# Kernel optimization log

Hardware: AMD Instinct MI355X
Metric: run time of the kernel (lower is better)

## Reference

```python
import jax, jax.numpy as jnp
import numpy as np

N = 50000        # num_nodes = user + item
D = 128          # latdim
L = 3            # gnn layers
R = 16           # hyper_rank
E = 1600000      # nnz of ts_drp_adj


def setup_inputs() -> dict:
    key = jax.random.key(0)
    ks = jax.random.split(key, 13)
    s = 1.0 / np.sqrt(D)
    return {
        "adj_rows": jax.random.randint(ks[0], (E,), 0, N, dtype=jnp.int32),
        "adj_cols": jax.random.randint(ks[1], (E,), 0, N, dtype=jnp.int32),
        "adj_vals": jax.random.uniform(ks[2], (E,), jnp.float32) * 0.05,
        "node_feats": jax.random.normal(ks[3], (N, D), jnp.float32) * s,
        "gnn_W": jax.random.normal(ks[4], (L, D, D), jnp.float32) * s,
        "gnn_b": jax.random.normal(ks[5], (L, D), jnp.float32) * 0.01,
        "fc1_W": jax.random.normal(ks[6], (D, D), jnp.float32) * s,
        "fc1_b": jax.random.normal(ks[7], (D,), jnp.float32) * 0.01,
        "fcrow_W": jax.random.normal(ks[8], (N * R, D), jnp.float32) * s,
        "fcrow_b": jax.random.normal(ks[9], (N * R,), jnp.float32) * 0.01,
        "fccol_W": jax.random.normal(ks[10], (R * D, D), jnp.float32) * s,
        "fccol_b": jax.random.normal(ks[11], (R * D,), jnp.float32) * 0.01,
        "ini_embeds": jax.random.normal(ks[12], (N, D), jnp.float32) * s,
    }


def _spmm(rows, cols, vals, h):
    # out[i] = sum_{e: rows[e]==i} vals[e] * h[cols[e]]   -- sparse adj @ h
    return jax.ops.segment_sum(vals[:, None] * h[cols], rows, num_segments=N)


def reference(adj_rows, adj_cols, adj_vals, node_feats, gnn_W, gnn_b,
              fc1_W, fc1_b, fcrow_W, fcrow_b, fccol_W, fccol_b, ini_embeds):
    h = node_feats
    h_sum = h  # running sum of layer outputs (residual mean-pool)
    for l in range(L):
        agg = _spmm(adj_rows, adj_cols, adj_vals, h)           # (N, D)
        h = jax.nn.elu(agg @ gnn_W[l].T + gnn_b[l])            # linear + ELU
        h_sum = h_sum + h
    h_bar = h_sum / (L + 1)
    z = h_bar.mean(axis=0)                                     # (D,)
    # Hypernetwork: z -> low-rank W_u = W_row @ W_col
    hz = jax.nn.leaky_relu(z @ fc1_W.T + fc1_b, negative_slope=0.2)
    W_row = (hz @ fcrow_W.T + fcrow_b).reshape(N, R)
    W_col = (hz @ fccol_W.T + fccol_b).reshape(R, D)
    W_u = W_row @ W_col                                        # (N, D)
    tuned_emb = ini_embeds + W_u * ini_embeds
    return tuned_emb
```

## Files before the change

kernel.cpp:

```cpp
#include <hip/hip_runtime.h>
#include <hip/hip_bf16.h>
#include <math.h>

#define NN 50000
#define DD 128
#define LLAYERS 3
#define RR 16
#define EE 1600000

typedef unsigned int u32;

__device__ __forceinline__ float bflo(u32 u){ union{u32 i;float f;}a; a.i=u<<16; return a.f; }
__device__ __forceinline__ float bfhi(u32 u){ union{u32 i;float f;}a; a.i=u&0xffff0000u; return a.f; }
__device__ __forceinline__ u32 pack_bf2(float x, float y){
  union{float f;u32 i;}a,b; a.f=x; b.f=y;
  u32 xr = (a.i + 0x7fffu + ((a.i>>16)&1u)) >> 16;
  u32 yr = (b.i + 0x7fffu + ((b.i>>16)&1u)) & 0xffff0000u;
  return (xr & 0xffffu) | yr;
}

__global__ __launch_bounds__(256) void k_hist(const int* __restrict__ rows, int* __restrict__ cnt){
  int e = blockIdx.x*256 + threadIdx.x;
  if (e < EE) atomicAdd(&cnt[rows[e]], 1);
}

__global__ __launch_bounds__(256) void k_scanA(const int* __restrict__ cnt, int* __restrict__ bsum){
  __shared__ int s[256];
  int i = blockIdx.x*256 + threadIdx.x;
  int v = (i < NN) ? cnt[i] : 0;
  s[threadIdx.x] = v; __syncthreads();
  for (int off=128; off>0; off>>=1){
    if (threadIdx.x < off) s[threadIdx.x] += s[threadIdx.x+off];
    __syncthreads();
  }
  if (threadIdx.x==0) bsum[blockIdx.x] = s[0];
}

__global__ __launch_bounds__(256) void k_scanB(int* bsum){
  __shared__ int s[256];
  int t = threadIdx.x;
  int v = bsum[t];
  s[t] = v; __syncthreads();
  for (int off=1; off<256; off<<=1){
    int x = (t>=off) ? s[t-off] : 0; __syncthreads();
    s[t] += x; __syncthreads();
  }
  bsum[t] = s[t] - v;
}

__global__ __launch_bounds__(256) void k_scanC(const int* __restrict__ cnt, const int* __restrict__ bsum,
                        int* __restrict__ row_ptr, int* __restrict__ cursor){
  __shared__ int s[256];
  int t = threadIdx.x; int i = blockIdx.x*256 + t;
  int v = (i<NN)?cnt[i]:0;
  s[t]=v; __syncthreads();
  for (int off=1; off<256; off<<=1){
    int x=(t>=off)?s[t-off]:0; __syncthreads();
    s[t]+=x; __syncthreads();
  }
  if (i<NN){ int e = bsum[blockIdx.x] + s[t]-v; row_ptr[i]=e; cursor[i]=e; }
}

__global__ __launch_bounds__(256) void k_scatter(const int* __restrict__ rows, const int* __restrict__ cols,
                          const float* __restrict__ vals,
                          int* __restrict__ cursor, int2* __restrict__ colval){
  int e = blockIdx.x*256+threadIdx.x;
  if (e<EE){
    int r = rows[e];
    int p = atomicAdd(&cursor[r],1);
    int2 cv; cv.x = cols[e]; cv.y = __float_as_int(vals[e]);
    colval[p] = cv;
  }
}

__global__ __launch_bounds__(256) void k_init(const float4* __restrict__ nf, uint2* __restrict__ hbf,
                                              float* __restrict__ z){
  __shared__ float zp[128];
  int t = threadIdx.x;
  if (t < 128) zp[t] = 0.f;
  float a0=0.f,a1=0.f,a2=0.f,a3=0.f;
  for (int i = blockIdx.x*256 + t; i < NN*DD/4; i += gridDim.x*256){
    float4 v = nf[i];
    uint2 p; p.x = pack_bf2(v.x, v.y); p.y = pack_bf2(v.z, v.w);
    hbf[i] = p;
    a0 += v.x; a1 += v.y; a2 += v.z; a3 += v.w;
  }
  __syncthreads();
  int c = (t*4) & 127;
  atomicAdd(&zp[c],a0); atomicAdd(&zp[c+1],a1); atomicAdd(&zp[c+2],a2); atomicAdd(&zp[c+3],a3);
  __syncthreads();
  if (t < 128) atomicAdd(&z[((blockIdx.x&15)<<7) + t], zp[t]);
}

__global__ __launch_bounds__(256) void k_wT(const float* __restrict__ W, float* __restrict__ wT){
  int idx = blockIdx.x*256+threadIdx.x;
  int l = idx >> 14; int r = idx & 16383; int k = r >> 7; int j = r & 127;
  wT[(l<<14) + k*128 + j] = W[(l<<14) + j*128 + k];
}

__global__ __launch_bounds__(256) void k_layer(const int* __restrict__ row_ptr, const int* __restrict__ cnt,
                       const int2* __restrict__ colval,
                       const u32* __restrict__ hin, const float* __restrict__ wTl,
                       const float* __restrict__ bl,
                       u32* __restrict__ hout, float* __restrict__ z, int last){
  __shared__ float a_s[16*128];
  __shared__ float zp[128];
  int t = threadIdx.x;
  if (t < 128) zp[t] = 0.f;
  int i0 = blockIdx.x * 16;
  int lane = t & 63;
  int wv = t >> 6;
  int sub = lane >> 4, k = lane & 15;

  for (int r = 0; r < 4; ++r){
    int row = i0 + wv*4 + r;
    int base = row_ptr[row], n = cnt[row];
    float a0=0,a1=0,a2=0,a3=0,a4=0,a5=0,a6=0,a7=0;
    int p = sub;
    for (; p + 4 < n; p += 8){
      int2 cv0 = colval[base+p];
      int2 cv1 = colval[base+p+4];
      uint4 h0 = *(const uint4*)&hin[((size_t)(u32)cv0.x<<6) + (k<<2)];
      uint4 h1 = *(const uint4*)&hin[((size_t)(u32)cv1.x<<6) + (k<<2)];
      float v0 = __int_as_float(cv0.y);
      float v1 = __int_as_float(cv1.y);
      a0 = fmaf(v0, bflo(h0.x), a0); a1 = fmaf(v0, bfhi(h0.x), a1);
      a2 = fmaf(v0, bflo(h0.y), a2); a3 = fmaf(v0, bfhi(h0.y), a3);
      a4 = fmaf(v0, bflo(h0.z), a4); a5 = fmaf(v0, bfhi(h0.z), a5);
      a6 = fmaf(v0, bflo(h0.w), a6); a7 = fmaf(v0, bfhi(h0.w), a7);
      a0 = fmaf(v1, bflo(h1.x), a0); a1 = fmaf(v1, bfhi(h1.x), a1);
      a2 = fmaf(v1, bflo(h1.y), a2); a3 = fmaf(v1, bfhi(h1.y), a3);
      a4 = fmaf(v1, bflo(h1.z), a4); a5 = fmaf(v1, bfhi(h1.z), a5);
      a6 = fmaf(v1, bflo(h1.w), a6); a7 = fmaf(v1, bfhi(h1.w), a7);
    }
    if (p < n){
      int2 cv = colval[base+p];
      float v = __int_as_float(cv.y);
      uint4 hv = *(const uint4*)&hin[((size_t)(u32)cv.x<<6) + (k<<2)];
      a0 = fmaf(v, bflo(hv.x), a0); a1 = fmaf(v, bfhi(hv.x), a1);
      a2 = fmaf(v, bflo(hv.y), a2); a3 = fmaf(v, bfhi(hv.y), a3);
      a4 = fmaf(v, bflo(hv.z), a4); a5 = fmaf(v, bfhi(hv.z), a5);
      a6 = fmaf(v, bflo(hv.w), a6); a7 = fmaf(v, bfhi(hv.w), a7);
    }
    a0 += __shfl_xor(a0,16); a0 += __shfl_xor(a0,32);
    a1 += __shfl_xor(a1,16); a1 += __shfl_xor(a1,32);
    a2 += __shfl_xor(a2,16); a2 += __shfl_xor(a2,32);
    a3 += __shfl_xor(a3,16); a3 += __shfl_xor(a3,32);
    a4 += __shfl_xor(a4,16); a4 += __shfl_xor(a4,32);
    a5 += __shfl_xor(a5,16); a5 += __shfl_xor(a5,32);
    a6 += __shfl_xor(a6,16); a6 += __shfl_xor(a6,32);
    a7 += __shfl_xor(a7,16); a7 += __shfl_xor(a7,32);
    if (sub==0){
      float4 o0; o0.x=a0; o0.y=a1; o0.z=a2; o0.w=a3;
      float4 o1; o1.x=a4; o1.y=a5; o1.z=a6; o1.w=a7;
      *(float4*)&a_s[(wv*4+r)*128 + k*8] = o0;
      *(float4*)&a_s[(wv*4+r)*128 + k*8 + 4] = o1;
    }
  }
  __syncthreads();

  int jj = lane*2;
  float b0 = bl[jj], b1 = bl[jj+1];
  float acc[4][2];
  #pragma unroll
  for (int r=0;r<4;r++){ acc[r][0]=b0; acc[r][1]=b1; }
  #pragma unroll 4
  for (int kk=0;kk<128;kk++){
    float2 w2 = *(const float2*)&wTl[kk*128 + jj];
    #pragma unroll
    for (int r=0;r<4;r++){
      float a = a_s[(wv*4+r)*128 + kk];
      acc[r][0] = fmaf(a, w2.x, acc[r][0]);
      acc[r][1] = fmaf(a, w2.y, acc[r][1]);
    }
  }
  float zc0 = 0.f, zc1 = 0.f;
  #pragma unroll
  for (int r=0;r<4;r++){
    int row = i0 + wv*4 + r;
    float e0 = acc[r][0] > 0.f ? acc[r][0] : expm1f(acc[r][0]);
    float e1 = acc[r][1] > 0.f ? acc[r][1] : expm1f(acc[r][1]);
    zc0 += e0; zc1 += e1;
    if (!last)
      hout[(size_t)row*64 + (jj>>1)] = pack_bf2(e0, e1);
  }
  atomicAdd(&zp[jj], zc0); atomicAdd(&zp[jj+1], zc1);
  __syncthreads();
  if (t < 128) atomicAdd(&z[((blockIdx.x&15)<<7) + t], zp[t]);
}

__global__ __launch_bounds__(128) void k_hz(const float* __restrict__ z, const float* __restrict__ fc1W,
                     const float* __restrict__ fc1b, float* __restrict__ hz){
  __shared__ float zs[128];
  int j = threadIdx.x;
  float s = 0.f;
  #pragma unroll
  for (int q=0;q<16;q++) s += z[(q<<7) + j];
  zs[j] = s * (1.0f / (4.0f * (float)NN));
  __syncthreads();
  float acc = fc1b[j];
  const float* wr = &fc1W[j*128];
  #pragma unroll 8
  for (int k=0;k<128;k++)
    acc = fmaf(zs[k], wr[k], acc);
  hz[j] = acc >= 0.f ? acc : 0.2f*acc;
}

__global__ __launch_bounds__(256) void k_wcol(const float* __restrict__ hz, const float* __restrict__ W,
                       const float* __restrict__ b, float* __restrict__ wcol){
  __shared__ float hzs[128];
  int t = threadIdx.x;
  if (t < 128) hzs[t] = hz[t];
  __syncthreads();
  int m = blockIdx.x*256 + t;
  float acc = b[m];
  const float* wr = &W[(size_t)m*128];
  #pragma unroll 8
  for (int k=0;k<128;k++)
    acc = fmaf(hzs[k], wr[k], acc);
  wcol[m] = acc;
}

__global__ __launch_bounds__(256) void k_wrow(const float* __restrict__ hz, const float* __restrict__ W,
                       const float* __restrict__ b, float* __restrict__ wrow){
  int lane = threadIdx.x & 63;
  int sub = lane >> 5, k = lane & 31;
  float4 hk = *(const float4*)&hz[k*4];
  int wid = (blockIdx.x*blockDim.x + threadIdx.x) >> 6;
  int nw = (gridDim.x*blockDim.x) >> 6;
  const int NITER = NN*RR/2;
  for (int it = wid; it < NITER; it += nw){
    int row = it*2 + sub;
    float4 wv = *(const float4*)&W[(size_t)row*128 + k*4];
    float acc = wv.x*hk.x;
    acc = fmaf(wv.y, hk.y, acc);
    acc = fmaf(wv.z, hk.z, acc);
    acc = fmaf(wv.w, hk.w, acc);
    acc += __shfl_xor(acc,1); acc += __shfl_xor(acc,2);
    acc += __shfl_xor(acc,4); acc += __shfl_xor(acc,8);
    acc += __shfl_xor(acc,16);
    if (k==0) wrow[row] = acc + b[row];
  }
}

__global__ __launch_bounds__(256) void k_final(const float* __restrict__ ini, const float* __restrict__ wrow,
                        const float* __restrict__ wcol, float* __restrict__ out){
  __shared__ float wc[16*128];
  int t = threadIdx.x;
  ((float4*)wc)[t] = ((const float4*)wcol)[t];
  ((float4*)wc)[t+256] = ((const float4*)wcol)[t+256];
  __syncthreads();
  int gid = blockIdx.x*256 + t;
  int i = gid >> 5, k = gid & 31;
  float4 a; a.x=0.f; a.y=0.f; a.z=0.f; a.w=0.f;
  const float* wri = &wrow[(size_t)i*16];
  #pragma unroll
  for (int r=0;r<16;r++){
    float w = wri[r];
    const float4 c = *(const float4*)&wc[r*128 + k*4];
    a.x = fmaf(w, c.x, a.x); a.y = fmaf(w, c.y, a.y);
    a.z = fmaf(w, c.z, a.z); a.w = fmaf(w, c.w, a.w);
  }
  float4 e = *(const float4*)&ini[(size_t)i*128 + k*4];
  float4 o;
  o.x = e.x*(1.f+a.x); o.y = e.y*(1.f+a.y);
  o.z = e.z*(1.f+a.z); o.w = e.w*(1.f+a.w);
  *(float4*)&out[(size_t)i*128 + k*4] = o;
}

extern "C" void kernel_launch(void* const* d_in, const int* in_sizes, int n_in,
                              void* d_out, int out_size, void* d_ws, size_t ws_size,
                              hipStream_t stream) {
  const int* adj_rows = (const int*)d_in[0];
  const int* adj_cols = (const int*)d_in[1];
  const float* adj_vals = (const float*)d_in[2];
  const float* node_feats = (const float*)d_in[3];
  const float* gnn_W = (const float*)d_in[4];
  const float* gnn_b = (const float*)d_in[5];
  const float* fc1_W = (const float*)d_in[6];
  const float* fc1_b = (const float*)d_in[7];
  const float* fcrow_W = (const float*)d_in[8];
  const float* fcrow_b = (const float*)d_in[9];
  const float* fccol_W = (const float*)d_in[10];
  const float* fccol_b = (const float*)d_in[11];
  const float* ini = (const float*)d_in[12];
  float* out = (float*)d_out;

  char* w = (char*)d_ws;
  auto alloc = [&](size_t bytes)->void*{ void* p = (void*)w; w += (bytes + 255) & ~(size_t)255; return p; };
  u32*   hbf_a  = (u32*)  alloc((size_t)NN*DD*2);
  u32*   hbf_b  = (u32*)  alloc((size_t)NN*DD*2);
  int2*  colval = (int2*) alloc((size_t)EE*8);
  int*   cnt    = (int*)  alloc((size_t)NN*4);
  int*   row_ptr= (int*)  alloc((size_t)NN*4);
  int*   cursor = (int*)  alloc((size_t)NN*4);
  int*   bsum   = (int*)  alloc(256*4);
  float* wT     = (float*)alloc(3*128*128*4);
  float* zb     = (float*)alloc(16*128*4);
  float* hzb    = (float*)alloc(128*4);
  float* wcolb  = (float*)alloc(2048*4);
  float* wrowb  = (float*)alloc((size_t)NN*RR*4);

  hipMemsetAsync(cnt, 0, NN*4, stream);
  hipMemsetAsync(zb, 0, 16*128*4, stream);

  k_hist<<<EE/256, 256, 0, stream>>>(adj_rows, cnt);
  k_scanA<<<256, 256, 0, stream>>>(cnt, bsum);
  k_scanB<<<1, 256, 0, stream>>>(bsum);
  k_scanC<<<256, 256, 0, stream>>>(cnt, bsum, row_ptr, cursor);
  k_scatter<<<EE/256, 256, 0, stream>>>(adj_rows, adj_cols, adj_vals, cursor, colval);
  k_init<<<400, 256, 0, stream>>>((const float4*)node_feats, (uint2*)hbf_a, zb);
  k_wT<<<3*128*128/256, 256, 0, stream>>>(gnn_W, wT);

  const u32* hin = hbf_a; u32* hout = hbf_b;
  for (int l=0; l<LLAYERS; ++l){
    k_layer<<<NN/16, 256, 0, stream>>>(row_ptr, cnt, colval, hin, wT + l*16384,
                                       gnn_b + l*128, hout, zb, (l==LLAYERS-1) ? 1 : 0);
    const u32* tmp = hin; hin = hout; hout = (u32*)tmp;
  }

  k_hz<<<1, 128, 0, stream>>>(zb, fc1_W, fc1_b, hzb);
  k_wcol<<<8, 256, 0, stream>>>(hzb, fccol_W, fccol_b, wcolb);
  k_wrow<<<2048, 256, 0, stream>>>(hzb, fcrow_W, fcrow_b, wrowb);
  k_final<<<NN*32/256, 256, 0, stream>>>(ini, wrowb, wcolb, out);
}
```

Measured before the change: 1.111 ms.

## Pad CSR rows to multiples of eight and software-pipeline SpMM gathers

Each row segment in the CSR arrays is padded to a multiple of 8 with zero-valued entries (column 0, value 0), plus a tail pad after the last row. The gather loop then needs no bounds check or remainder path. The inner SpMM loop is software-pipelined, prefetching colval two iterations ahead and feature rows one iteration ahead to hide gather latency. The cost is about 1.6x more colval storage at worst, an extra padding kernel, and wasted FMAs and gathers on padded slots.

```diff
diff --git a/kernel.cpp b/kernel.cpp
--- a/kernel.cpp
+++ b/kernel.cpp
@@ -27,7 +27,7 @@
 __global__ __launch_bounds__(256) void k_scanA(const int* __restrict__ cnt, int* __restrict__ bsum){
   __shared__ int s[256];
   int i = blockIdx.x*256 + threadIdx.x;
-  int v = (i < NN) ? cnt[i] : 0;
+  int v = (i < NN) ? ((cnt[i]+7)&~7) : 0;
   s[threadIdx.x] = v; __syncthreads();
   for (int off=128; off>0; off>>=1){
     if (threadIdx.x < off) s[threadIdx.x] += s[threadIdx.x+off];
@@ -52,13 +52,26 @@
                         int* __restrict__ row_ptr, int* __restrict__ cursor){
   __shared__ int s[256];
   int t = threadIdx.x; int i = blockIdx.x*256 + t;
-  int v = (i<NN)?cnt[i]:0;
+  int v = (i<NN)?((cnt[i]+7)&~7):0;
   s[t]=v; __syncthreads();
   for (int off=1; off<256; off<<=1){
     int x=(t>=off)?s[t-off]:0; __syncthreads();
     s[t]+=x; __syncthreads();
   }
   if (i<NN){ int e = bsum[blockIdx.x] + s[t]-v; row_ptr[i]=e; cursor[i]=e; }
+}
+
+__global__ __launch_bounds__(256) void k_pad(const int* __restrict__ row_ptr, const int* __restrict__ cnt,
+                                             int2* __restrict__ colval){
+  int i = blockIdx.x*256 + threadIdx.x;
+  if (i < NN){
+    int b = row_ptr[i], n = cnt[i], np = (n+7)&~7;
+    int2 z0; z0.x = 0; z0.y = 0;
+    for (int p=b+n; p<b+np; ++p) colval[p] = z0;
+    if (i == NN-1){
+      for (int p=b+np; p<b+np+128; ++p) colval[p] = z0;
+    }
+  }
 }
 
 __global__ __launch_bounds__(256) void k_scatter(const int* __restrict__ rows, const int* __restrict__ cols,
@@ -98,6 +111,12 @@
   wT[(l<<14) + k*128 + j] = W[(l<<14) + j*128 + k];
 }
 
+#define FMA8(v, h)                                         \
+  a0 = fmaf(v, bflo(h.x), a0); a1 = fmaf(v, bfhi(h.x), a1);\
+  a2 = fmaf(v, bflo(h.y), a2); a3 = fmaf(v, bfhi(h.y), a3);\
+  a4 = fmaf(v, bflo(h.z), a4); a5 = fmaf(v, bfhi(h.z), a5);\
+  a6 = fmaf(v, bflo(h.w), a6); a7 = fmaf(v, bfhi(h.w), a7);
+
 __global__ __launch_bounds__(256) void k_layer(const int* __restrict__ row_ptr, const int* __restrict__ cnt,
                        const int2* __restrict__ colval,
                        const u32* __restrict__ hin, const float* __restrict__ wTl,
@@ -115,33 +134,28 @@
   for (int r = 0; r < 4; ++r){
     int row = i0 + wv*4 + r;
     int base = row_ptr[row], n = cnt[row];
+    int iters = (n + 7) >> 3;
+    const int2* cvp = colval + base + sub;
     float a0=0,a1=0,a2=0,a3=0,a4=0,a5=0,a6=0,a7=0;
-    int p = sub;
-    for (; p + 4 < n; p += 8){
-      int2 cv0 = colval[base+p];
-      int2 cv1 = colval[base+p+4];
-      uint4 h0 = *(const uint4*)&hin[((size_t)(u32)cv0.x<<6) + (k<<2)];
-      uint4 h1 = *(const uint4*)&hin[((size_t)(u32)cv1.x<<6) + (k<<2)];
-      float v0 = __int_as_float(cv0.y);
-      float v1 = __int_as_float(cv1.y);
-      a0 = fmaf(v0, bflo(h0.x), a0); a1 = fmaf(v0, bfhi(h0.x), a1);
-      a2 = fmaf(v0, bflo(h0.y), a2); a3 = fmaf(v0, bfhi(h0.y), a3);
-      a4 = fmaf(v0, bflo(h0.z), a4); a5 = fmaf(v0, bfhi(h0.z), a5);
-      a6 = fmaf(v0, bflo(h0.w), a6); a7 = fmaf(v0, bfhi(h0.w), a7);
-      a0 = fmaf(v1, bflo(h1.x), a0); a1 = fmaf(v1, bfhi(h1.x), a1);
-      a2 = fmaf(v1, bflo(h1.y), a2); a3 = fmaf(v1, bfhi(h1.y), a3);
-      a4 = fmaf(v1, bflo(h1.z), a4); a5 = fmaf(v1, bfhi(h1.z), a5);
-      a6 = fmaf(v1, bflo(h1.w), a6); a7 = fmaf(v1, bfhi(h1.w), a7);
+
+    int2 c0a = cvp[0],  c0b = cvp[4];
+    int2 c1a = cvp[8],  c1b = cvp[12];
+    uint4 h0a = *(const uint4*)&hin[((size_t)(u32)c0a.x<<6) + (k<<2)];
+    uint4 h0b = *(const uint4*)&hin[((size_t)(u32)c0b.x<<6) + (k<<2)];
+
+    for (int it = 0; it < iters; ++it){
+      int2 c2a = cvp[16], c2b = cvp[20];
+      uint4 h1a = *(const uint4*)&hin[((size_t)(u32)c1a.x<<6) + (k<<2)];
+      uint4 h1b = *(const uint4*)&hin[((size_t)(u32)c1b.x<<6) + (k<<2)];
+      float v0 = __int_as_float(c0a.y);
+      float v1 = __int_as_float(c0b.y);
+      FMA8(v0, h0a);
+      FMA8(v1, h0b);
+      c0a = c1a; c0b = c1b; c1a = c2a; c1b = c2b;
+      h0a = h1a; h0b = h1b;
+      cvp += 8;
     }
-    if (p < n){
-      int2 cv = colval[base+p];
-      float v = __int_as_float(cv.y);
-      uint4 hv = *(const uint4*)&hin[((size_t)(u32)cv.x<<6) + (k<<2)];
-      a0 = fmaf(v, bflo(hv.x), a0); a1 = fmaf(v, bfhi(hv.x), a1);
-      a2 = fmaf(v, bflo(hv.y), a2); a3 = fmaf(v, bfhi(hv.y), a3);
-      a4 = fmaf(v, bflo(hv.z), a4); a5 = fmaf(v, bfhi(hv.z), a5);
-      a6 = fmaf(v, bflo(hv.w), a6); a7 = fmaf(v, bfhi(hv.w), a7);
-    }
+
     a0 += __shfl_xor(a0,16); a0 += __shfl_xor(a0,32);
     a1 += __shfl_xor(a1,16); a1 += __shfl_xor(a1,32);
     a2 += __shfl_xor(a2,16); a2 += __shfl_xor(a2,32);
@@ -290,7 +304,7 @@
   auto alloc = [&](size_t bytes)->void*{ void* p = (void*)w; w += (bytes + 255) & ~(size_t)255; return p; };
   u32*   hbf_a  = (u32*)  alloc((size_t)NN*DD*2);
   u32*   hbf_b  = (u32*)  alloc((size_t)NN*DD*2);
-  int2*  colval = (int2*) alloc((size_t)EE*8);
+  int2*  colval = (int2*) alloc(((size_t)EE + 8*NN + 256)*8);
   int*   cnt    = (int*)  alloc((size_t)NN*4);
   int*   row_ptr= (int*)  alloc((size_t)NN*4);
   int*   cursor = (int*)  alloc((size_t)NN*4);
@@ -308,6 +322,7 @@
   k_scanA<<<256, 256, 0, stream>>>(cnt, bsum);
   k_scanB<<<1, 256, 0, stream>>>(bsum);
   k_scanC<<<256, 256, 0, stream>>>(cnt, bsum, row_ptr, cursor);
+  k_pad<<<(NN+255)/256, 256, 0, stream>>>(row_ptr, cnt, colval);
   k_scatter<<<EE/256, 256, 0, stream>>>(adj_rows, adj_cols, adj_vals, cursor, colval);
   k_init<<<400, 256, 0, stream>>>((const float4*)node_feats, (uint2*)hbf_a, zb);
   k_wT<<<3*128*128/256, 256, 0, stream>>>(gnn_W, wT);
```

New measurement: 1.094 ms. No clear change (-1.6%).
